# Kernel tuning notes

Hardware: AMD Instinct MI355X
Metric: run time of the kernel (lower is better)

The kernel has to match this reference:

```python
import jax, jax.numpy as jnp
import numpy as np

B, S = 64, 128
NQ, C = 2000, 128
K, DE, DC = 64, 64, 64


def _glorot(k, shape):
    lim = float(np.sqrt(6.0 / (shape[0] + shape[1])))
    return jax.random.uniform(k, shape, jnp.float32, -lim, lim)


def setup_inputs() -> dict:
    key = jax.random.key(0)
    ks = jax.random.split(key, 16)
    return {
        'question_seq': jax.random.randint(ks[0], (B, S), 0, NQ, dtype=jnp.int32),
        'correctness_seq': jax.random.randint(ks[1], (B, S), 0, 2, dtype=jnp.int32),
        'q_matrix': (jax.random.uniform(ks[2], (NQ, C)) < 0.15).astype(jnp.float32),
        'E_q': jax.random.normal(ks[3], (NQ, DE), jnp.float32) * 0.02,
        'E_c': jax.random.normal(ks[4], (2, DC), jnp.float32) * 0.02,
        'h0': _glorot(ks[5], (C, K)),
        'W1': _glorot(ks[6], (DC + DE, K)), 'b1': jnp.zeros((K,), jnp.float32),
        'W2': _glorot(ks[7], (3 * K, K)), 'b2': jnp.zeros((K,), jnp.float32),
        'W3': _glorot(ks[8], (3 * K, K)), 'b3': jnp.zeros((K,), jnp.float32),
        'W4': _glorot(ks[9], (2 * K, K)), 'b4': jnp.zeros((K,), jnp.float32),
        'Wab': _glorot(ks[10], (K, 1)), 'bab': jnp.zeros((1,), jnp.float32),
        'Wdiff': _glorot(ks[11], (DE, C)), 'bdiff': jnp.zeros((C,), jnp.float32),
        'Wdisc': _glorot(ks[12], (DE, 1)), 'bdisc': jnp.zeros((1,), jnp.float32),
    }


def _forward(question_seq, correctness_seq, q_matrix, E_q, E_c, h0,
             W1, b1, W2, b2, W3, b3, W4, b4,
             Wab, bab, Wdiff, bdiff, Wdisc, bdisc):
    e_emb = E_q[question_seq]                 # [B,S,DE]
    c_emb = E_c[correctness_seq]              # [B,S,DC]
    all_learning = jnp.concatenate([e_emb, c_emb], -1) @ W1 + b1  # [B,S,K]
    q_seq = q_matrix[question_seq]            # [B,S,C]

    h_pre0 = jnp.broadcast_to(h0, (B, C, K))
    h_tilde0 = jnp.einsum('bc,ck->bk', q_seq[:, 0], h0)
    learning0 = jnp.zeros((B, K), jnp.float32)

    xs = (
        jnp.moveaxis(q_seq[:, :-1], 1, 0),        # q_e        [S-1,B,C]
        jnp.moveaxis(all_learning[:, :-1], 1, 0),  # learning   [S-1,B,K]
        jnp.moveaxis(q_seq[:, 1:], 1, 0),         # q_next     [S-1,B,C]
        jnp.moveaxis(e_emb[:, 1:], 1, 0),         # e_next     [S-1,B,DE]
    )

    def step(carry, x):
        h_pre, h_tilde_pre, learning_pre = carry
        q_e, learning, q_next, e_next = x
        cat = jnp.concatenate([learning_pre, learning, h_tilde_pre], -1)  # [B,3K]
        learning_gain = jnp.tanh(cat @ W2 + b2)
        gamma_l = jax.nn.sigmoid(cat @ W3 + b3)
        LG = gamma_l * (learning_gain + 1.0) * 0.5                       # [B,K]
        LG_tilde = q_e[:, :, None] * LG[:, None, :]                      # [B,C,K] rank-1 scatter
        gate_in = jnp.concatenate(
            [h_pre, jnp.broadcast_to(LG[:, None, :], (B, C, K))], -1)    # [B,C,2K]
        gamma_f = jax.nn.sigmoid(gate_in @ W4 + b4)
        h = LG_tilde + gamma_f * h_pre                                   # [B,C,K]
        ability = jax.nn.sigmoid(jnp.squeeze(h @ Wab + bab, -1)) * q_next  # [B,C]
        diff = jax.nn.sigmoid(e_next @ Wdiff + bdiff) * q_next             # [B,C]
        disc = jax.nn.sigmoid(e_next @ Wdisc + bdisc) * 5.0                # [B,1]
        y = jax.nn.sigmoid(jnp.sum(disc * (ability - diff), -1))          # [B]
        h_tilde = jnp.einsum('bc,bck->bk', q_next, h)
        return (h, h_tilde, learning), y

    _, ys = jax.lax.scan(step, (h_pre0, h_tilde0, learning0), xs)  # ys [S-1,B]
    pred = jnp.concatenate([jnp.zeros((B, 1), jnp.float32), ys.T], axis=1)  # [B,S]
    return pred


def reference(question_seq, correctness_seq, q_matrix, E_q, E_c, h0,
              W1, b1, W2, b2, W3, b3, W4, b4,
              Wab, bab, Wdiff, bdiff, Wdisc, bdisc):
    return _forward(question_seq, correctness_seq, q_matrix, E_q, E_c, h0,
                    W1, b1, W2, b2, W3, b3, W4, b4,
                    Wab, bab, Wdiff, bdiff, Wdisc, bdisc)
```

## Files before the change

kernel.cpp:

```cpp
#include <hip/hip_runtime.h>


constexpr int BB = 64, SS = 128, CD = 128;
constexpr int RECF = 136;
constexpr int HP2  = 72;

typedef short bf16x8 __attribute__((ext_vector_type(8)));
typedef float f32x4  __attribute__((ext_vector_type(4)));

#define BAR() asm volatile("s_waitcnt lgkmcnt(0)\ns_barrier" ::: "memory")

__device__ __forceinline__ short f2bf(float x) {
  unsigned u = __builtin_bit_cast(unsigned, x);
  unsigned r = u + 0x7fffu + ((u >> 16) & 1u);
  return (short)(r >> 16);
}
__device__ __forceinline__ unsigned pk2bf(float a, float b) {
  unsigned ua = __builtin_bit_cast(unsigned, a);
  unsigned ub = __builtin_bit_cast(unsigned, b);
  unsigned ra = ua + 0x7fffu + ((ua >> 16) & 1u);
  unsigned rb = ub + 0x7fffu + ((ub >> 16) & 1u);
  return (ra >> 16) | (rb & 0xffff0000u);
}
__device__ __forceinline__ float sigm(float x) {
  return __builtin_amdgcn_rcpf(1.f + __expf(-x));
}
__device__ __forceinline__ void store_bf4(short* p, float a, float b, float c, float d) {
  uint2 v = {pk2bf(a, b), pk2bf(c, d)};
  *(uint2*)p = v;
}

__global__ void pcT(const float* __restrict__ Eq, const float* __restrict__ qmat,
                    const float* __restrict__ W1, const float* __restrict__ W2,
                    const float* __restrict__ W3, const float* __restrict__ Ec,
                    const float* __restrict__ b1,
                    const float* __restrict__ Wdiff, const float* __restrict__ bdiff,
                    const float* __restrict__ Wdisc, const float* __restrict__ bdisc,
                    float* __restrict__ T, float* __restrict__ DIFF,
                    float* __restrict__ DISCq, float* __restrict__ Uws) {
  int q0 = blockIdx.x * 8, tid = threadIdx.x;
  __shared__ float e[8][64], al[8][64];
  for (int i = tid; i < 512; i += 256) e[i >> 6][i & 63] = Eq[(q0 + (i >> 6)) * 64 + (i & 63)];
  __syncthreads();
  for (int i = tid; i < 512; i += 256) {
    int qq = i >> 6, k = i & 63;
    float s = 0.f;
    #pragma unroll 8
    for (int d = 0; d < 64; ++d) s += e[qq][d] * W1[d * 64 + k];
    al[qq][k] = s;
  }
  __syncthreads();
  {
    int m = tid >> 6, k = tid & 63;
    const float* src = (m < 2 ? W2 : W3) + (m & 1) * 64 * 64;
    float acc[8] = {0.f, 0.f, 0.f, 0.f, 0.f, 0.f, 0.f, 0.f};
    for (int j = 0; j < 64; ++j) {
      float w = src[j * 64 + k];
      #pragma unroll
      for (int qq = 0; qq < 8; ++qq) acc[qq] += al[qq][j] * w;
    }
    #pragma unroll
    for (int qq = 0; qq < 8; ++qq) T[(q0 + qq) * 256 + m * 64 + k] = acc[qq];
  }
  if (tid < 128) {
    int c = tid;
    float acc[8] = {0.f, 0.f, 0.f, 0.f, 0.f, 0.f, 0.f, 0.f};
    for (int d = 0; d < 64; ++d) {
      float w = Wdiff[d * 128 + c];
      #pragma unroll
      for (int qq = 0; qq < 8; ++qq) acc[qq] += e[qq][d] * w;
    }
    #pragma unroll
    for (int qq = 0; qq < 8; ++qq)
      DIFF[(q0 + qq) * 128 + c] = qmat[(q0 + qq) * 128 + c] * sigm(acc[qq] + bdiff[c]);
  } else if (tid < 136) {
    int qq = tid - 128;
    float s = 0.f;
    for (int d = 0; d < 64; ++d) s += e[qq][d] * Wdisc[d];
    DISCq[q0 + qq] = 5.f * sigm(s + bdisc[0]);
  }
  if (blockIdx.x == 0) {
    __shared__ float alc[2][64];
    if (tid < 128) {
      int cr = tid >> 6, k = tid & 63;
      float s = b1[k];
      for (int d = 0; d < 64; ++d) s += Ec[cr * 64 + d] * W1[(64 + d) * 64 + k];
      alc[cr][k] = s;
    }
    __syncthreads();
    if (tid < 128) {
      int cr = tid >> 6, k = tid & 63;
      float u2a = 0.f, u2b = 0.f, u3a = 0.f, u3b = 0.f;
      for (int j = 0; j < 64; ++j) {
        float a = alc[cr][j];
        u2a += a * W2[j * 64 + k];       u2b += a * W2[(64 + j) * 64 + k];
        u3a += a * W3[j * 64 + k];       u3b += a * W3[(64 + j) * 64 + k];
      }
      Uws[(0 + cr) * 64 + k] = u2a;  Uws[(2 + cr) * 64 + k] = u2b;
      Uws[(4 + cr) * 64 + k] = u3a;  Uws[(6 + cr) * 64 + k] = u3b;
    }
  }
}

__global__ void pcR(const int* __restrict__ qs, const int* __restrict__ cs,
                    const float* __restrict__ qmat,
                    const float* __restrict__ b2, const float* __restrict__ b3,
                    const float* __restrict__ T, const float* __restrict__ Uws,
                    float* __restrict__ REC) {
  int tid = threadIdx.x;
  for (int i = 0; i < 4; ++i) {
    int bs = blockIdx.x * 4 + i;
    int t  = bs & (SS - 1);
    int q_t = qs[bs];
    float* rec = REC + (size_t)bs * RECF;
    if (tid < 64) {
      int k = tid;
      float v2 = b2[k], v3 = b3[k];
      if (t >= 1) {
        int q1 = qs[bs - 1], c1 = cs[bs - 1];
        v2 += T[q1 * 256 + 64 + k]  + Uws[(2 + c1) * 64 + k];
        v3 += T[q1 * 256 + 192 + k] + Uws[(6 + c1) * 64 + k];
      }
      if (t >= 2) {
        int q2 = qs[bs - 2], c2 = cs[bs - 2];
        v2 += T[q2 * 256 + k]       + Uws[(0 + c2) * 64 + k];
        v3 += T[q2 * 256 + 128 + k] + Uws[(4 + c2) * 64 + k];
      }
      int pp = (k & 15) * 4 + (k >> 4);
      rec[pp] = v2; rec[64 + pp] = v3;
    }
    unsigned long long m = __ballot(qmat[q_t * 128 + tid] > 0.5f);
    int wv = tid >> 6, lane = tid & 63;
    if (lane == 0) {
      rec[128 + wv * 2]     = __uint_as_float((unsigned)m);
      rec[128 + wv * 2 + 1] = __uint_as_float((unsigned)(m >> 32));
    }
  }
}

__global__ void pcY(const int* __restrict__ qs, const float* __restrict__ qmat,
                    const float* __restrict__ DIFF, const float* __restrict__ DISCq,
                    const float* __restrict__ YP, const float* __restrict__ bab,
                    float* __restrict__ out) {
  int tid = threadIdx.x, lane = tid & 63, wv = tid >> 6;
  const float bab0 = bab[0];
  __shared__ float red[4][2];
  #pragma unroll
  for (int i = 0; i < 4; ++i) {
    int bs = blockIdx.x * 4 + i;
    int t  = bs & (SS - 1);
    float v = 0.f;
    if (t != 0) {
      int q_t = qs[bs];
      float yp = YP[(size_t)bs * 128 + tid];
      float qn = qmat[q_t * 128 + tid] > 0.5f ? 1.f : 0.f;
      v = sigm(yp + bab0) * qn - DIFF[q_t * 128 + tid];
    }
    v += __shfl_xor(v, 32); v += __shfl_xor(v, 16); v += __shfl_xor(v, 8);
    v += __shfl_xor(v, 4);  v += __shfl_xor(v, 2);  v += __shfl_xor(v, 1);
    if (lane == 0) red[i][wv] = v;
  }
  __syncthreads();
  if (tid < 4) {
    int bs = blockIdx.x * 4 + tid;
    int t  = bs & (SS - 1);
    if (t == 0) out[bs] = 0.f;
    else        out[bs] = sigm(DISCq[qs[bs]] * (red[tid][0] + red[tid][1]));
  }
}

__global__ __launch_bounds__(256, 1) __attribute__((amdgpu_waves_per_eu(1, 1)))
void lpkt_main(
    const float* __restrict__ h0,
    const float* __restrict__ W2, const float* __restrict__ W3,
    const float* __restrict__ W4, const float* __restrict__ b4,
    const float* __restrict__ Wab,
    const float* __restrict__ REC, float* __restrict__ YP) {
  __shared__ __align__(16) short hsb[CD * HP2];
  __shared__ __align__(16) short lgb[4 * 64];
  __shared__ __align__(16) short pkb[4 * 64];
  __shared__ __align__(16) float up[2][4][2][64];

  const int b    = blockIdx.x;
  const int tid  = threadIdx.x;
  const int lane = tid & 63;
  const int wv   = tid >> 6;
  const int col  = lane & 15;
  const int quad = lane >> 4;
  const int bS   = b * SS;
  const f32x4 zz = {0.f, 0.f, 0.f, 0.f};

  const float* W4a = W4;
  const float* W4b = W4 + 64 * 64;
  const float* W2c = W2 + 128 * 64;
  const float* W3c = W3 + 128 * 64;

  bf16x8 bw4[4][2], bwb[4][2], bw2[4][2], bw3[4][2], bwab[2];
  float b4r[4];
  #pragma unroll
  for (int nb = 0; nb < 4; ++nb) {
    #pragma unroll
    for (int half = 0; half < 2; ++half)
      #pragma unroll
      for (int j = 0; j < 8; ++j) {
        int p  = half * 32 + quad * 8 + j;
        int ke = (p & 3) * 16 + (p >> 2);
        int kk = ke * 64 + nb * 16 + col;
        bw4[nb][half][j] = f2bf(W4a[kk]);
        bwb[nb][half][j] = f2bf(W4b[kk]);
        bw2[nb][half][j] = f2bf(W2c[kk]);
        bw3[nb][half][j] = f2bf(W3c[kk]);
      }
    b4r[nb] = b4[nb * 16 + col];
  }
  #pragma unroll
  for (int half = 0; half < 2; ++half)
    #pragma unroll
    for (int j = 0; j < 8; ++j) {
      int p  = half * 32 + quad * 8 + j;
      int ke = (p & 3) * 16 + (p >> 2);
      bwab[half][j] = (col == 0) ? f2bf(Wab[ke]) : (short)0;
    }

  float h2[2][4][4];
  #pragma unroll
  for (int mt = 0; mt < 2; ++mt)
    #pragma unroll
    for (int reg = 0; reg < 4; ++reg) {
      int c = 32 * wv + 16 * mt + 4 * quad + reg;
      #pragma unroll
      for (int n = 0; n < 4; ++n) h2[mt][reg][n] = h0[c * 64 + n * 16 + col];
      store_bf4(&hsb[c * HP2 + col * 4],
                h2[mt][reg][0], h2[mt][reg][1], h2[mt][reg][2], h2[mt][reg][3]);
    }

  unsigned qe_w = __float_as_uint(REC[(size_t)bS * RECF + 128 + wv]);
  {
    float pk[4] = {0.f, 0.f, 0.f, 0.f};
    #pragma unroll
    for (int mt = 0; mt < 2; ++mt)
      #pragma unroll
      for (int reg = 0; reg < 4; ++reg) {
        float q = (float)((qe_w >> (16 * mt + 4 * quad + reg)) & 1u);
        #pragma unroll
        for (int n = 0; n < 4; ++n) pk[n] += q * h2[mt][reg][n];
      }
    #pragma unroll
    for (int n = 0; n < 4; ++n) {
      pk[n] += __shfl_xor(pk[n], 16);
      pk[n] += __shfl_xor(pk[n], 32);
    }
    if (quad == 0) store_bf4(&pkb[wv * 64 + col * 4], pk[0], pk[1], pk[2], pk[3]);
  }
  bf16x8 pf0 = *(const bf16x8*)&pkb[wv * 64 + quad * 8];
  bf16x8 pf1 = *(const bf16x8*)&pkb[wv * 64 + 32 + quad * 8];
  {
    float v2[4], v3[4];
    #pragma unroll
    for (int nb = 0; nb < 4; ++nb) {
      f32x4 a2 = __builtin_amdgcn_mfma_f32_16x16x32_bf16(pf0, bw2[nb][0], zz, 0, 0, 0);
      a2 = __builtin_amdgcn_mfma_f32_16x16x32_bf16(pf1, bw2[nb][1], a2, 0, 0, 0);
      f32x4 a3 = __builtin_amdgcn_mfma_f32_16x16x32_bf16(pf0, bw3[nb][0], zz, 0, 0, 0);
      a3 = __builtin_amdgcn_mfma_f32_16x16x32_bf16(pf1, bw3[nb][1], a3, 0, 0, 0);
      v2[nb] = a2[0]; v3[nb] = a3[0];
    }
    if (quad == 0) {
      *(float4*)&up[1][wv][0][col * 4] = make_float4(v2[0], v2[1], v2[2], v2[3]);
      *(float4*)&up[1][wv][1][col * 4] = make_float4(v3[0], v3[1], v3[2], v3[3]);
    }
  }
  bf16x8 af[2][2];
  #pragma unroll
  for (int mt = 0; mt < 2; ++mt) {
    int r = 32 * wv + 16 * mt + col;
    af[mt][0] = *(const bf16x8*)&hsb[r * HP2 + quad * 8];
    af[mt][1] = *(const bf16x8*)&hsb[r * HP2 + 32 + quad * 8];
  }
  f32x4 acc[2][4];
  #pragma unroll
  for (int mt = 0; mt < 2; ++mt)
    #pragma unroll
    for (int nb = 0; nb < 4; ++nb) {
      acc[mt][nb] = __builtin_amdgcn_mfma_f32_16x16x32_bf16(af[mt][0], bw4[nb][0], zz, 0, 0, 0);
      acc[mt][nb] = __builtin_amdgcn_mfma_f32_16x16x32_bf16(af[mt][1], bw4[nb][1], acc[mt][nb], 0, 0, 0);
    }

  unsigned qbw[2];
  qbw[1] = __float_as_uint(REC[(size_t)(bS + 1) * RECF + 128 + wv]);
  qbw[0] = __float_as_uint(REC[(size_t)(bS + 2) * RECF + 128 + wv]);
  float4 pb2[2], pb3[2];
  pb2[1] = *(const float4*)&REC[(size_t)(bS + 1) * RECF + col * 4];
  pb3[1] = *(const float4*)&REC[(size_t)(bS + 1) * RECF + 64 + col * 4];
  pb2[0] = *(const float4*)&REC[(size_t)(bS + 2) * RECF + col * 4];
  pb3[0] = *(const float4*)&REC[(size_t)(bS + 2) * RECF + 64 + col * 4];
  BAR();

  for (int t = 1; t < SS; ++t) {
    const int par = t & 1;
    float4 u2v = pb2[par], u3v = pb3[par];
    {
      float4 a0 = *(const float4*)&up[par][0][0][col * 4];
      float4 a1 = *(const float4*)&up[par][1][0][col * 4];
      float4 a2 = *(const float4*)&up[par][2][0][col * 4];
      float4 a3 = *(const float4*)&up[par][3][0][col * 4];
      float4 c0 = *(const float4*)&up[par][0][1][col * 4];
      float4 c1 = *(const float4*)&up[par][1][1][col * 4];
      float4 c2 = *(const float4*)&up[par][2][1][col * 4];
      float4 c3 = *(const float4*)&up[par][3][1][col * 4];
      u2v.x += a0.x + a1.x + a2.x + a3.x;  u3v.x += c0.x + c1.x + c2.x + c3.x;
      u2v.y += a0.y + a1.y + a2.y + a3.y;  u3v.y += c0.y + c1.y + c2.y + c3.y;
      u2v.z += a0.z + a1.z + a2.z + a3.z;  u3v.z += c0.z + c1.z + c2.z + c3.z;
      u2v.w += a0.w + a1.w + a2.w + a3.w;  u3v.w += c0.w + c1.w + c2.w + c3.w;
    }
    float lg[4];
    lg[0] = sigm(u3v.x) * sigm(2.f * u2v.x);
    lg[1] = sigm(u3v.y) * sigm(2.f * u2v.y);
    lg[2] = sigm(u3v.z) * sigm(2.f * u2v.z);
    lg[3] = sigm(u3v.w) * sigm(2.f * u2v.w);
    if (quad == 0) store_bf4(&lgb[wv * 64 + col * 4], lg[0], lg[1], lg[2], lg[3]);
    unsigned qn_w = qbw[par];
    {
      int tn = (t + 2 < SS) ? t + 2 : SS - 1;
      const float* rn = REC + (size_t)(bS + tn) * RECF;
      qbw[par] = __float_as_uint(rn[128 + wv]);
      pb2[par] = *(const float4*)&rn[col * 4];
      pb3[par] = *(const float4*)&rn[64 + col * 4];
    }
    bf16x8 lf0 = *(const bf16x8*)&lgb[wv * 64 + quad * 8];
    bf16x8 lf1 = *(const bf16x8*)&lgb[wv * 64 + 32 + quad * 8];
    float tvv[4];
    #pragma unroll
    for (int nb = 0; nb < 4; ++nb) {
      f32x4 bb = __builtin_amdgcn_mfma_f32_16x16x32_bf16(lf0, bwb[nb][0], zz, 0, 0, 0);
      bb = __builtin_amdgcn_mfma_f32_16x16x32_bf16(lf1, bwb[nb][1], bb, 0, 0, 0);
      tvv[nb] = bb[0] + b4r[nb];
    }
    #pragma unroll
    for (int mt = 0; mt < 2; ++mt)
      #pragma unroll
      for (int reg = 0; reg < 4; ++reg) {
        int c = 32 * wv + 16 * mt + 4 * quad + reg;
        float qe = (float)((qe_w >> (16 * mt + 4 * quad + reg)) & 1u);
        #pragma unroll
        for (int nb = 0; nb < 4; ++nb) {
          float g = sigm(acc[mt][nb][reg] + tvv[nb]);
          h2[mt][reg][nb] = qe * lg[nb] + g * h2[mt][reg][nb];
        }
        store_bf4(&hsb[c * HP2 + col * 4],
                  h2[mt][reg][0], h2[mt][reg][1], h2[mt][reg][2], h2[mt][reg][3]);
      }
    {
      float pk[4] = {0.f, 0.f, 0.f, 0.f};
      #pragma unroll
      for (int mt = 0; mt < 2; ++mt)
        #pragma unroll
        for (int reg = 0; reg < 4; ++reg) {
          float q = (float)((qn_w >> (16 * mt + 4 * quad + reg)) & 1u);
          #pragma unroll
          for (int n = 0; n < 4; ++n) pk[n] += q * h2[mt][reg][n];
        }
      #pragma unroll
      for (int n = 0; n < 4; ++n) {
        pk[n] += __shfl_xor(pk[n], 16);
        pk[n] += __shfl_xor(pk[n], 32);
      }
      if (quad == 0) store_bf4(&pkb[wv * 64 + col * 4], pk[0], pk[1], pk[2], pk[3]);
    }
    pf0 = *(const bf16x8*)&pkb[wv * 64 + quad * 8];
    pf1 = *(const bf16x8*)&pkb[wv * 64 + 32 + quad * 8];
    {
      float v2[4], v3[4];
      #pragma unroll
      for (int nb = 0; nb < 4; ++nb) {
        f32x4 a2 = __builtin_amdgcn_mfma_f32_16x16x32_bf16(pf0, bw2[nb][0], zz, 0, 0, 0);
        a2 = __builtin_amdgcn_mfma_f32_16x16x32_bf16(pf1, bw2[nb][1], a2, 0, 0, 0);
        f32x4 a3 = __builtin_amdgcn_mfma_f32_16x16x32_bf16(pf0, bw3[nb][0], zz, 0, 0, 0);
        a3 = __builtin_amdgcn_mfma_f32_16x16x32_bf16(pf1, bw3[nb][1], a3, 0, 0, 0);
        v2[nb] = a2[0]; v3[nb] = a3[0];
      }
      if (quad == 0) {
        *(float4*)&up[par ^ 1][wv][0][col * 4] = make_float4(v2[0], v2[1], v2[2], v2[3]);
        *(float4*)&up[par ^ 1][wv][1][col * 4] = make_float4(v3[0], v3[1], v3[2], v3[3]);
      }
    }
    #pragma unroll
    for (int mt = 0; mt < 2; ++mt) {
      int r = 32 * wv + 16 * mt + col;
      af[mt][0] = *(const bf16x8*)&hsb[r * HP2 + quad * 8];
      af[mt][1] = *(const bf16x8*)&hsb[r * HP2 + 32 + quad * 8];
    }
    #pragma unroll
    for (int mt = 0; mt < 2; ++mt)
      #pragma unroll
      for (int nb = 0; nb < 4; ++nb) {
        acc[mt][nb] = __builtin_amdgcn_mfma_f32_16x16x32_bf16(af[mt][0], bw4[nb][0], zz, 0, 0, 0);
        acc[mt][nb] = __builtin_amdgcn_mfma_f32_16x16x32_bf16(af[mt][1], bw4[nb][1], acc[mt][nb], 0, 0, 0);
      }
    #pragma unroll
    for (int mt = 0; mt < 2; ++mt) {
      f32x4 ya = __builtin_amdgcn_mfma_f32_16x16x32_bf16(af[mt][0], bwab[0], zz, 0, 0, 0);
      ya = __builtin_amdgcn_mfma_f32_16x16x32_bf16(af[mt][1], bwab[1], ya, 0, 0, 0);
      if (col == 0)
        *(float4*)&YP[((size_t)bS + t) * 128 + 32 * wv + 16 * mt + 4 * quad]
            = make_float4(ya[0], ya[1], ya[2], ya[3]);
    }
    qe_w = qn_w;
    BAR();
  }
}

extern "C" void kernel_launch(void* const* d_in, const int* in_sizes, int n_in,
                              void* d_out, int out_size, void* d_ws, size_t ws_size,
                              hipStream_t stream) {
  const int*   qs    = (const int*)d_in[0];
  const int*   cs    = (const int*)d_in[1];
  const float* qmat  = (const float*)d_in[2];
  const float* Eq    = (const float*)d_in[3];
  const float* Ec    = (const float*)d_in[4];
  const float* h0    = (const float*)d_in[5];
  const float* W1    = (const float*)d_in[6];
  const float* b1    = (const float*)d_in[7];
  const float* W2    = (const float*)d_in[8];
  const float* b2    = (const float*)d_in[9];
  const float* W3    = (const float*)d_in[10];
  const float* b3    = (const float*)d_in[11];
  const float* W4    = (const float*)d_in[12];
  const float* b4    = (const float*)d_in[13];
  const float* Wab   = (const float*)d_in[14];
  const float* bab   = (const float*)d_in[15];
  const float* Wdiff = (const float*)d_in[16];
  const float* bdiff = (const float*)d_in[17];
  const float* Wdisc = (const float*)d_in[18];
  const float* bdisc = (const float*)d_in[19];
  float* out = (float*)d_out;

  float* w = (float*)d_ws;
  float* T     = w;
  float* DIFF  = T + 512000;
  float* DISCq = DIFF + 256000;
  float* Uws   = DISCq + 2000;
  float* REC   = Uws + 512;
  float* YP    = REC + (size_t)BB * SS * RECF;

  pcT<<<250, 256, 0, stream>>>(Eq, qmat, W1, W2, W3, Ec, b1, Wdiff, bdiff, Wdisc, bdisc,
                               T, DIFF, DISCq, Uws);
  pcR<<<BB * SS / 4, 128, 0, stream>>>(qs, cs, qmat, b2, b3, T, Uws, REC);
  lpkt_main<<<BB, 256, 0, stream>>>(h0, W2, W3, W4, b4, Wab, REC, YP);
  pcY<<<BB * SS / 4, 128, 0, stream>>>(qs, qmat, DIFF, DISCq, YP, bab, out);
}
```

Measured before the change: 365.1 us.

## Fuse record-building and output kernels into the recurrent main kernel

Removes the pcR and pcY kernels. Per-step bias/projection records are now assembled inside the recurrent loop from the permuted T table, a per-question bitmask table and register-held Uws values, prefetched one step ahead. The final prediction reduction runs as an epilogue of the main kernel, which cuts two launches and the REC buffer traffic. In exchange the serial loop does more gather loads and adds per step, and the epilogue runs on only 64 blocks.

```diff
diff --git a/kernel.cpp b/kernel.cpp
--- a/kernel.cpp
+++ b/kernel.cpp
@@ -2,8 +2,7 @@
 
 
 constexpr int BB = 64, SS = 128, CD = 128;
-constexpr int RECF = 136;
-constexpr int HP2  = 72;
+constexpr int HP2 = 72;
 
 typedef short bf16x8 __attribute__((ext_vector_type(8)));
 typedef float f32x4  __attribute__((ext_vector_type(4)));
@@ -29,15 +28,23 @@
   uint2 v = {pk2bf(a, b), pk2bf(c, d)};
   *(uint2*)p = v;
 }
+__device__ __forceinline__ float4 f4add(float4 a, float4 b) {
+  return make_float4(a.x + b.x, a.y + b.y, a.z + b.z, a.w + b.w);
+}
+__device__ __forceinline__ float4 f4sel(float4 a, float4 b, int c) {
+  return c ? b : a;
+}
 
 __global__ void pcT(const float* __restrict__ Eq, const float* __restrict__ qmat,
                     const float* __restrict__ W1, const float* __restrict__ W2,
                     const float* __restrict__ W3, const float* __restrict__ Ec,
-                    const float* __restrict__ b1,
+                    const float* __restrict__ b1, const float* __restrict__ b2,
+                    const float* __restrict__ b3,
                     const float* __restrict__ Wdiff, const float* __restrict__ bdiff,
                     const float* __restrict__ Wdisc, const float* __restrict__ bdisc,
-                    float* __restrict__ T, float* __restrict__ DIFF,
-                    float* __restrict__ DISCq, float* __restrict__ Uws) {
+                    float* __restrict__ Tp, float* __restrict__ DIFF,
+                    float* __restrict__ DISCq, float* __restrict__ Uwsp,
+                    unsigned* __restrict__ QB) {
   int q0 = blockIdx.x * 8, tid = threadIdx.x;
   __shared__ float e[8][64], al[8][64];
   for (int i = tid; i < 512; i += 256) e[i >> 6][i & 63] = Eq[(q0 + (i >> 6)) * 64 + (i & 63)];
@@ -52,6 +59,7 @@
   __syncthreads();
   {
     int m = tid >> 6, k = tid & 63;
+    int pp = (k & 15) * 4 + (k >> 4);
     const float* src = (m < 2 ? W2 : W3) + (m & 1) * 64 * 64;
     float acc[8] = {0.f, 0.f, 0.f, 0.f, 0.f, 0.f, 0.f, 0.f};
     for (int j = 0; j < 64; ++j) {
@@ -60,7 +68,7 @@
       for (int qq = 0; qq < 8; ++qq) acc[qq] += al[qq][j] * w;
     }
     #pragma unroll
-    for (int qq = 0; qq < 8; ++qq) T[(q0 + qq) * 256 + m * 64 + k] = acc[qq];
+    for (int qq = 0; qq < 8; ++qq) Tp[(q0 + qq) * 256 + m * 64 + pp] = acc[qq];
   }
   if (tid < 128) {
     int c = tid;
@@ -73,6 +81,15 @@
     #pragma unroll
     for (int qq = 0; qq < 8; ++qq)
       DIFF[(q0 + qq) * 128 + c] = qmat[(q0 + qq) * 128 + c] * sigm(acc[qq] + bdiff[c]);
+    int w = tid >> 6, lane = tid & 63;
+    #pragma unroll
+    for (int qq = 0; qq < 8; ++qq) {
+      unsigned long long m = __ballot(qmat[(q0 + qq) * 128 + c] > 0.5f);
+      if (lane == 0) {
+        QB[(q0 + qq) * 4 + w * 2]     = (unsigned)m;
+        QB[(q0 + qq) * 4 + w * 2 + 1] = (unsigned)(m >> 32);
+      }
+    }
   } else if (tid < 136) {
     int qq = tid - 128;
     float s = 0.f;
@@ -90,82 +107,16 @@
     __syncthreads();
     if (tid < 128) {
       int cr = tid >> 6, k = tid & 63;
+      int pp = (k & 15) * 4 + (k >> 4);
       float u2a = 0.f, u2b = 0.f, u3a = 0.f, u3b = 0.f;
       for (int j = 0; j < 64; ++j) {
         float a = alc[cr][j];
         u2a += a * W2[j * 64 + k];       u2b += a * W2[(64 + j) * 64 + k];
         u3a += a * W3[j * 64 + k];       u3b += a * W3[(64 + j) * 64 + k];
       }
-      Uws[(0 + cr) * 64 + k] = u2a;  Uws[(2 + cr) * 64 + k] = u2b;
-      Uws[(4 + cr) * 64 + k] = u3a;  Uws[(6 + cr) * 64 + k] = u3b;
-    }
-  }
-}
-
-__global__ void pcR(const int* __restrict__ qs, const int* __restrict__ cs,
-                    const float* __restrict__ qmat,
-                    const float* __restrict__ b2, const float* __restrict__ b3,
-                    const float* __restrict__ T, const float* __restrict__ Uws,
-                    float* __restrict__ REC) {
-  int tid = threadIdx.x;
-  for (int i = 0; i < 4; ++i) {
-    int bs = blockIdx.x * 4 + i;
-    int t  = bs & (SS - 1);
-    int q_t = qs[bs];
-    float* rec = REC + (size_t)bs * RECF;
-    if (tid < 64) {
-      int k = tid;
-      float v2 = b2[k], v3 = b3[k];
-      if (t >= 1) {
-        int q1 = qs[bs - 1], c1 = cs[bs - 1];
-        v2 += T[q1 * 256 + 64 + k]  + Uws[(2 + c1) * 64 + k];
-        v3 += T[q1 * 256 + 192 + k] + Uws[(6 + c1) * 64 + k];
-      }
-      if (t >= 2) {
-        int q2 = qs[bs - 2], c2 = cs[bs - 2];
-        v2 += T[q2 * 256 + k]       + Uws[(0 + c2) * 64 + k];
-        v3 += T[q2 * 256 + 128 + k] + Uws[(4 + c2) * 64 + k];
-      }
-      int pp = (k & 15) * 4 + (k >> 4);
-      rec[pp] = v2; rec[64 + pp] = v3;
-    }
-    unsigned long long m = __ballot(qmat[q_t * 128 + tid] > 0.5f);
-    int wv = tid >> 6, lane = tid & 63;
-    if (lane == 0) {
-      rec[128 + wv * 2]     = __uint_as_float((unsigned)m);
-      rec[128 + wv * 2 + 1] = __uint_as_float((unsigned)(m >> 32));
-    }
-  }
-}
-
-__global__ void pcY(const int* __restrict__ qs, const float* __restrict__ qmat,
-                    const float* __restrict__ DIFF, const float* __restrict__ DISCq,
-                    const float* __restrict__ YP, const float* __restrict__ bab,
-                    float* __restrict__ out) {
-  int tid = threadIdx.x, lane = tid & 63, wv = tid >> 6;
-  const float bab0 = bab[0];
-  __shared__ float red[4][2];
-  #pragma unroll
-  for (int i = 0; i < 4; ++i) {
-    int bs = blockIdx.x * 4 + i;
-    int t  = bs & (SS - 1);
-    float v = 0.f;
-    if (t != 0) {
-      int q_t = qs[bs];
-      float yp = YP[(size_t)bs * 128 + tid];
-      float qn = qmat[q_t * 128 + tid] > 0.5f ? 1.f : 0.f;
-      v = sigm(yp + bab0) * qn - DIFF[q_t * 128 + tid];
-    }
-    v += __shfl_xor(v, 32); v += __shfl_xor(v, 16); v += __shfl_xor(v, 8);
-    v += __shfl_xor(v, 4);  v += __shfl_xor(v, 2);  v += __shfl_xor(v, 1);
-    if (lane == 0) red[i][wv] = v;
-  }
-  __syncthreads();
-  if (tid < 4) {
-    int bs = blockIdx.x * 4 + tid;
-    int t  = bs & (SS - 1);
-    if (t == 0) out[bs] = 0.f;
-    else        out[bs] = sigm(DISCq[qs[bs]] * (red[tid][0] + red[tid][1]));
+      Uwsp[(0 + cr) * 64 + pp] = u2a;  Uwsp[(2 + cr) * 64 + pp] = u2b + b2[k];
+      Uwsp[(4 + cr) * 64 + pp] = u3a;  Uwsp[(6 + cr) * 64 + pp] = u3b + b3[k];
+    }
   }
 }
 
@@ -174,12 +125,17 @@
     const float* __restrict__ h0,
     const float* __restrict__ W2, const float* __restrict__ W3,
     const float* __restrict__ W4, const float* __restrict__ b4,
-    const float* __restrict__ Wab,
-    const float* __restrict__ REC, float* __restrict__ YP) {
+    const float* __restrict__ Wab, const float* __restrict__ bab,
+    const int* __restrict__ qs, const int* __restrict__ cs,
+    const float* __restrict__ Tp, const float* __restrict__ Uwsp,
+    const unsigned* __restrict__ QB,
+    const float* __restrict__ DIFF, const float* __restrict__ DISCq,
+    float* __restrict__ YP, float* __restrict__ out) {
   __shared__ __align__(16) short hsb[CD * HP2];
   __shared__ __align__(16) short lgb[4 * 64];
   __shared__ __align__(16) short pkb[4 * 64];
   __shared__ __align__(16) float up[2][4][2][64];
+  __shared__ int qsl[SS], csl[SS];
 
   const int b    = blockIdx.x;
   const int tid  = threadIdx.x;
@@ -195,6 +151,9 @@
   const float* W2c = W2 + 128 * 64;
   const float* W3c = W3 + 128 * 64;
 
+  if (tid < 128) qsl[tid] = qs[bS + tid];
+  else           csl[tid - 128] = cs[bS + tid - 128];
+
   bf16x8 bw4[4][2], bwb[4][2], bw2[4][2], bw3[4][2], bwab[2];
   float b4r[4];
   #pragma unroll
@@ -222,6 +181,15 @@
       bwab[half][j] = (col == 0) ? f2bf(Wab[ke]) : (short)0;
     }
 
+  float4 rU2a[2], rU2b[2], rU3a[2], rU3b[2];
+  #pragma unroll
+  for (int cr = 0; cr < 2; ++cr) {
+    rU2a[cr] = *(const float4*)&Uwsp[(0 + cr) * 64 + col * 4];
+    rU2b[cr] = *(const float4*)&Uwsp[(2 + cr) * 64 + col * 4];
+    rU3a[cr] = *(const float4*)&Uwsp[(4 + cr) * 64 + col * 4];
+    rU3b[cr] = *(const float4*)&Uwsp[(6 + cr) * 64 + col * 4];
+  }
+
   float h2[2][4][4];
   #pragma unroll
   for (int mt = 0; mt < 2; ++mt)
@@ -234,7 +202,8 @@
                 h2[mt][reg][0], h2[mt][reg][1], h2[mt][reg][2], h2[mt][reg][3]);
     }
 
-  unsigned qe_w = __float_as_uint(REC[(size_t)bS * RECF + 128 + wv]);
+  int q0i = qs[bS], c0i = cs[bS];
+  unsigned qe_w = QB[q0i * 4 + wv];
   {
     float pk[4] = {0.f, 0.f, 0.f, 0.f};
     #pragma unroll
@@ -285,19 +254,29 @@
       acc[mt][nb] = __builtin_amdgcn_mfma_f32_16x16x32_bf16(af[mt][1], bw4[nb][1], acc[mt][nb], 0, 0, 0);
     }
 
+  float4 pbF2, pbF3;
+  {
+    float4 t2b = *(const float4*)&Tp[q0i * 256 + 64 + col * 4];
+    float4 t3b = *(const float4*)&Tp[q0i * 256 + 192 + col * 4];
+    pbF2 = f4add(t2b, f4sel(rU2b[0], rU2b[1], c0i));
+    pbF3 = f4add(t3b, f4sel(rU3b[0], rU3b[1], c0i));
+  }
+  float4 rT2b, rT2a, rT3b, rT3a;
+  {
+    int q1 = qs[bS + 1];
+    rT2b = *(const float4*)&Tp[q1 * 256 + 64 + col * 4];
+    rT3b = *(const float4*)&Tp[q1 * 256 + 192 + col * 4];
+    rT2a = *(const float4*)&Tp[q0i * 256 + col * 4];
+    rT3a = *(const float4*)&Tp[q0i * 256 + 128 + col * 4];
+  }
   unsigned qbw[2];
-  qbw[1] = __float_as_uint(REC[(size_t)(bS + 1) * RECF + 128 + wv]);
-  qbw[0] = __float_as_uint(REC[(size_t)(bS + 2) * RECF + 128 + wv]);
-  float4 pb2[2], pb3[2];
-  pb2[1] = *(const float4*)&REC[(size_t)(bS + 1) * RECF + col * 4];
-  pb3[1] = *(const float4*)&REC[(size_t)(bS + 1) * RECF + 64 + col * 4];
-  pb2[0] = *(const float4*)&REC[(size_t)(bS + 2) * RECF + col * 4];
-  pb3[0] = *(const float4*)&REC[(size_t)(bS + 2) * RECF + 64 + col * 4];
+  qbw[1] = QB[qs[bS + 1] * 4 + wv];
+  qbw[0] = QB[qs[bS + 2] * 4 + wv];
   BAR();
 
   for (int t = 1; t < SS; ++t) {
     const int par = t & 1;
-    float4 u2v = pb2[par], u3v = pb3[par];
+    float4 u2v = pbF2, u3v = pbF3;
     {
       float4 a0 = *(const float4*)&up[par][0][0][col * 4];
       float4 a1 = *(const float4*)&up[par][1][0][col * 4];
@@ -319,13 +298,6 @@
     lg[3] = sigm(u3v.w) * sigm(2.f * u2v.w);
     if (quad == 0) store_bf4(&lgb[wv * 64 + col * 4], lg[0], lg[1], lg[2], lg[3]);
     unsigned qn_w = qbw[par];
-    {
-      int tn = (t + 2 < SS) ? t + 2 : SS - 1;
-      const float* rn = REC + (size_t)(bS + tn) * RECF;
-      qbw[par] = __float_as_uint(rn[128 + wv]);
-      pb2[par] = *(const float4*)&rn[col * 4];
-      pb3[par] = *(const float4*)&rn[64 + col * 4];
-    }
     bf16x8 lf0 = *(const bf16x8*)&lgb[wv * 64 + quad * 8];
     bf16x8 lf1 = *(const bf16x8*)&lgb[wv * 64 + 32 + quad * 8];
     float tvv[4];
@@ -404,8 +376,45 @@
         *(float4*)&YP[((size_t)bS + t) * 128 + 32 * wv + 16 * mt + 4 * quad]
             = make_float4(ya[0], ya[1], ya[2], ya[3]);
     }
+    if (t < SS - 1) {
+      int cc1 = csl[t], cc2 = csl[t - 1];
+      pbF2 = f4add(f4add(rT2b, rT2a),
+                   f4add(f4sel(rU2b[0], rU2b[1], cc1), f4sel(rU2a[0], rU2a[1], cc2)));
+      pbF3 = f4add(f4add(rT3b, rT3a),
+                   f4add(f4sel(rU3b[0], rU3b[1], cc1), f4sel(rU3a[0], rU3a[1], cc2)));
+      int tn = (t + 2 < SS) ? t + 2 : SS - 1;
+      int qq1 = qsl[t + 1], qq2 = qsl[t];
+      rT2b = *(const float4*)&Tp[qq1 * 256 + 64 + col * 4];
+      rT3b = *(const float4*)&Tp[qq1 * 256 + 192 + col * 4];
+      rT2a = *(const float4*)&Tp[qq2 * 256 + col * 4];
+      rT3a = *(const float4*)&Tp[qq2 * 256 + 128 + col * 4];
+      qbw[par] = QB[qsl[tn] * 4 + wv];
+    }
     qe_w = qn_w;
     BAR();
+  }
+
+  asm volatile("s_waitcnt vmcnt(0)" ::: "memory");
+  __syncthreads();
+  const float bab0 = bab[0];
+  if (tid == 0) out[bS] = 0.f;
+  #pragma unroll 2
+  for (int i = 0; i < 32; ++i) {
+    int t = wv * 32 + i;
+    if (t == 0) continue;
+    int qt = qsl[t];
+    float yp0 = YP[((size_t)bS + t) * 128 + lane];
+    float yp1 = YP[((size_t)bS + t) * 128 + 64 + lane];
+    float d0  = DIFF[qt * 128 + lane];
+    float d1  = DIFF[qt * 128 + 64 + lane];
+    unsigned w0 = QB[qt * 4 + (lane >> 5)];
+    unsigned w1 = QB[qt * 4 + 2 + (lane >> 5)];
+    float qa = (float)((w0 >> (lane & 31)) & 1u);
+    float qb = (float)((w1 >> (lane & 31)) & 1u);
+    float v = sigm(yp0 + bab0) * qa - d0 + sigm(yp1 + bab0) * qb - d1;
+    v += __shfl_xor(v, 32); v += __shfl_xor(v, 16); v += __shfl_xor(v, 8);
+    v += __shfl_xor(v, 4);  v += __shfl_xor(v, 2);  v += __shfl_xor(v, 1);
+    if (lane == 0) out[bS + t] = sigm(DISCq[qt] * v);
   }
 }
 
@@ -435,16 +444,16 @@
   float* out = (float*)d_out;
 
   float* w = (float*)d_ws;
-  float* T     = w;
-  float* DIFF  = T + 512000;
-  float* DISCq = DIFF + 256000;
-  float* Uws   = DISCq + 2000;
-  float* REC   = Uws + 512;
-  float* YP    = REC + (size_t)BB * SS * RECF;
-
-  pcT<<<250, 256, 0, stream>>>(Eq, qmat, W1, W2, W3, Ec, b1, Wdiff, bdiff, Wdisc, bdisc,
-                               T, DIFF, DISCq, Uws);
-  pcR<<<BB * SS / 4, 128, 0, stream>>>(qs, cs, qmat, b2, b3, T, Uws, REC);
-  lpkt_main<<<BB, 256, 0, stream>>>(h0, W2, W3, W4, b4, Wab, REC, YP);
-  pcY<<<BB * SS / 4, 128, 0, stream>>>(qs, qmat, DIFF, DISCq, YP, bab, out);
-}
+  float*    Tpb   = w;
+  float*    DIFF  = Tpb + 512000;
+  float*    DISCq = DIFF + 256000;
+  float*    Uwsp  = DISCq + 2000;
+  unsigned* QB    = (unsigned*)(Uwsp + 512);
+  float*    YP    = (float*)(QB + 8000);
+
+  pcT<<<250, 256, 0, stream>>>(Eq, qmat, W1, W2, W3, Ec, b1, b2, b3,
+                               Wdiff, bdiff, Wdisc, bdisc,
+                               Tpb, DIFF, DISCq, Uwsp, QB);
+  lpkt_main<<<BB, 256, 0, stream>>>(h0, W2, W3, W4, b4, Wab, bab, qs, cs,
+                                    Tpb, Uwsp, QB, DIFF, DISCq, YP, out);
+}
```

Result: slower. 411.4 us (+12.7%).

## Fuse output kernel into recurrent kernel and replace LDS fragment staging with shuffles

Applied to the files above, without the earlier changes.

Removes the separate pcY launch and computes the final per-step prediction at the end of lpkt_main, reading the q-mask bits from the precomputed REC records instead of the q_matrix. Inside the recurrent loop, the LDS round trips used to turn per-column results (pk and lg) into MFMA A-fragments are replaced by cross-lane shuffles. This cuts a kernel launch and LDS traffic on the sequential critical path, at the cost of extra shuffle instructions and a serial epilogue that runs on only 64 blocks.

```diff
diff --git a/kernel.cpp b/kernel.cpp
--- a/kernel.cpp
+++ b/kernel.cpp
@@ -28,6 +28,16 @@
 __device__ __forceinline__ void store_bf4(short* p, float a, float b, float c, float d) {
   uint2 v = {pk2bf(a, b), pk2bf(c, d)};
   *(uint2*)p = v;
+}
+__device__ __forceinline__ void frag_from_cols(unsigned p0, unsigned p1, int quad,
+                                               bf16x8& f0, bf16x8& f1) {
+  int s0 = 2 * quad, s1 = s0 + 1, s2 = s0 + 8, s3 = s0 + 9;
+  uint4 a = {(unsigned)__shfl((int)p0, s0), (unsigned)__shfl((int)p1, s0),
+             (unsigned)__shfl((int)p0, s1), (unsigned)__shfl((int)p1, s1)};
+  uint4 b = {(unsigned)__shfl((int)p0, s2), (unsigned)__shfl((int)p1, s2),
+             (unsigned)__shfl((int)p0, s3), (unsigned)__shfl((int)p1, s3)};
+  f0 = __builtin_bit_cast(bf16x8, a);
+  f1 = __builtin_bit_cast(bf16x8, b);
 }
 
 __global__ void pcT(const float* __restrict__ Eq, const float* __restrict__ qmat,
@@ -138,48 +148,19 @@
   }
 }
 
-__global__ void pcY(const int* __restrict__ qs, const float* __restrict__ qmat,
-                    const float* __restrict__ DIFF, const float* __restrict__ DISCq,
-                    const float* __restrict__ YP, const float* __restrict__ bab,
-                    float* __restrict__ out) {
-  int tid = threadIdx.x, lane = tid & 63, wv = tid >> 6;
-  const float bab0 = bab[0];
-  __shared__ float red[4][2];
-  #pragma unroll
-  for (int i = 0; i < 4; ++i) {
-    int bs = blockIdx.x * 4 + i;
-    int t  = bs & (SS - 1);
-    float v = 0.f;
-    if (t != 0) {
-      int q_t = qs[bs];
-      float yp = YP[(size_t)bs * 128 + tid];
-      float qn = qmat[q_t * 128 + tid] > 0.5f ? 1.f : 0.f;
-      v = sigm(yp + bab0) * qn - DIFF[q_t * 128 + tid];
-    }
-    v += __shfl_xor(v, 32); v += __shfl_xor(v, 16); v += __shfl_xor(v, 8);
-    v += __shfl_xor(v, 4);  v += __shfl_xor(v, 2);  v += __shfl_xor(v, 1);
-    if (lane == 0) red[i][wv] = v;
-  }
-  __syncthreads();
-  if (tid < 4) {
-    int bs = blockIdx.x * 4 + tid;
-    int t  = bs & (SS - 1);
-    if (t == 0) out[bs] = 0.f;
-    else        out[bs] = sigm(DISCq[qs[bs]] * (red[tid][0] + red[tid][1]));
-  }
-}
-
 __global__ __launch_bounds__(256, 1) __attribute__((amdgpu_waves_per_eu(1, 1)))
 void lpkt_main(
     const float* __restrict__ h0,
     const float* __restrict__ W2, const float* __restrict__ W3,
     const float* __restrict__ W4, const float* __restrict__ b4,
-    const float* __restrict__ Wab,
-    const float* __restrict__ REC, float* __restrict__ YP) {
+    const float* __restrict__ Wab, const float* __restrict__ bab,
+    const int* __restrict__ qs,
+    const float* __restrict__ REC, const float* __restrict__ DIFF,
+    const float* __restrict__ DISCq,
+    float* __restrict__ YP, float* __restrict__ out) {
   __shared__ __align__(16) short hsb[CD * HP2];
-  __shared__ __align__(16) short lgb[4 * 64];
-  __shared__ __align__(16) short pkb[4 * 64];
   __shared__ __align__(16) float up[2][4][2][64];
+  __shared__ int qsl[SS];
 
   const int b    = blockIdx.x;
   const int tid  = threadIdx.x;
@@ -195,6 +176,8 @@
   const float* W2c = W2 + 128 * 64;
   const float* W3c = W3 + 128 * 64;
 
+  if (tid < 128) qsl[tid] = qs[bS + tid];
+
   bf16x8 bw4[4][2], bwb[4][2], bw2[4][2], bw3[4][2], bwab[2];
   float b4r[4];
   #pragma unroll
@@ -235,6 +218,7 @@
     }
 
   unsigned qe_w = __float_as_uint(REC[(size_t)bS * RECF + 128 + wv]);
+  bf16x8 pf0, pf1;
   {
     float pk[4] = {0.f, 0.f, 0.f, 0.f};
     #pragma unroll
@@ -250,10 +234,8 @@
       pk[n] += __shfl_xor(pk[n], 16);
       pk[n] += __shfl_xor(pk[n], 32);
     }
-    if (quad == 0) store_bf4(&pkb[wv * 64 + col * 4], pk[0], pk[1], pk[2], pk[3]);
-  }
-  bf16x8 pf0 = *(const bf16x8*)&pkb[wv * 64 + quad * 8];
-  bf16x8 pf1 = *(const bf16x8*)&pkb[wv * 64 + 32 + quad * 8];
+    frag_from_cols(pk2bf(pk[0], pk[1]), pk2bf(pk[2], pk[3]), quad, pf0, pf1);
+  }
   {
     float v2[4], v3[4];
     #pragma unroll
@@ -317,7 +299,8 @@
     lg[1] = sigm(u3v.y) * sigm(2.f * u2v.y);
     lg[2] = sigm(u3v.z) * sigm(2.f * u2v.z);
     lg[3] = sigm(u3v.w) * sigm(2.f * u2v.w);
-    if (quad == 0) store_bf4(&lgb[wv * 64 + col * 4], lg[0], lg[1], lg[2], lg[3]);
+    bf16x8 lf0, lf1;
+    frag_from_cols(pk2bf(lg[0], lg[1]), pk2bf(lg[2], lg[3]), quad, lf0, lf1);
     unsigned qn_w = qbw[par];
     {
       int tn = (t + 2 < SS) ? t + 2 : SS - 1;
@@ -326,8 +309,6 @@
       pb2[par] = *(const float4*)&rn[col * 4];
       pb3[par] = *(const float4*)&rn[64 + col * 4];
     }
-    bf16x8 lf0 = *(const bf16x8*)&lgb[wv * 64 + quad * 8];
-    bf16x8 lf1 = *(const bf16x8*)&lgb[wv * 64 + 32 + quad * 8];
     float tvv[4];
     #pragma unroll
     for (int nb = 0; nb < 4; ++nb) {
@@ -364,10 +345,8 @@
         pk[n] += __shfl_xor(pk[n], 16);
         pk[n] += __shfl_xor(pk[n], 32);
       }
-      if (quad == 0) store_bf4(&pkb[wv * 64 + col * 4], pk[0], pk[1], pk[2], pk[3]);
-    }
-    pf0 = *(const bf16x8*)&pkb[wv * 64 + quad * 8];
-    pf1 = *(const bf16x8*)&pkb[wv * 64 + 32 + quad * 8];
+      frag_from_cols(pk2bf(pk[0], pk[1]), pk2bf(pk[2], pk[3]), quad, pf0, pf1);
+    }
     {
       float v2[4], v3[4];
       #pragma unroll
@@ -406,6 +385,29 @@
     }
     qe_w = qn_w;
     BAR();
+  }
+
+  __syncthreads();
+  const float bab0 = bab[0];
+  if (tid == 0) out[bS] = 0.f;
+  #pragma unroll 2
+  for (int i = 0; i < 32; ++i) {
+    int t = wv * 32 + i;
+    if (t == 0) continue;
+    int qt = qsl[t];
+    const float* rec = REC + (size_t)(bS + t) * RECF;
+    float yp0 = YP[((size_t)bS + t) * 128 + lane];
+    float yp1 = YP[((size_t)bS + t) * 128 + 64 + lane];
+    float d0  = DIFF[qt * 128 + lane];
+    float d1  = DIFF[qt * 128 + 64 + lane];
+    unsigned w0 = __float_as_uint(rec[128 + (lane >> 5)]);
+    unsigned w1 = __float_as_uint(rec[130 + (lane >> 5)]);
+    float qa = (float)((w0 >> (lane & 31)) & 1u);
+    float qb = (float)((w1 >> (lane & 31)) & 1u);
+    float v = sigm(yp0 + bab0) * qa - d0 + sigm(yp1 + bab0) * qb - d1;
+    v += __shfl_xor(v, 32); v += __shfl_xor(v, 16); v += __shfl_xor(v, 8);
+    v += __shfl_xor(v, 4);  v += __shfl_xor(v, 2);  v += __shfl_xor(v, 1);
+    if (lane == 0) out[bS + t] = sigm(DISCq[qt] * v);
   }
 }
 
@@ -442,9 +444,9 @@
   float* REC   = Uws + 512;
   float* YP    = REC + (size_t)BB * SS * RECF;
 
-  pcT<<<250, 256, 0, stream>>>(Eq, qmat, W1, W2, W3, Ec, b1, Wdiff, bdiff, Wdisc, bdisc,
-                               T, DIFF, DISCq, Uws);
+  pcT<<<250, 256, 0, stream>>>(Eq, qmat, W1, W2, W3, Ec, b1,
+                               Wdiff, bdiff, Wdisc, bdisc, T, DIFF, DISCq, Uws);
   pcR<<<BB * SS / 4, 128, 0, stream>>>(qs, cs, qmat, b2, b3, T, Uws, REC);
-  lpkt_main<<<BB, 256, 0, stream>>>(h0, W2, W3, W4, b4, Wab, REC, YP);
-  pcY<<<BB * SS / 4, 128, 0, stream>>>(qs, qmat, DIFF, DISCq, YP, bab, out);
-}
+  lpkt_main<<<BB, 256, 0, stream>>>(h0, W2, W3, W4, b4, Wab, bab, qs,
+                                    REC, DIFF, DISCq, YP, out);
+}
```

Measured after the change: 483.5 us. 32.4% more time.
